# Performance work log

Hardware: AMD Instinct MI355X
Metric: run time of the kernel (lower is better)

## Reference

```python
import jax, jax.numpy as jnp
import numpy as np

DIM = 1024
N_HEADS = 16
WINDOW = 256
B, N = 16, 4096
ACC = 512
EPS = 1e-5


def setup_inputs() -> dict:
    key = jax.random.key(0)
    ks = jax.random.split(key, 16)
    D = DIM
    sc = 1.0 / np.sqrt(D)
    inp = {
        "x": jax.random.normal(ks[0], (B, N, D), dtype=jnp.float32),
        "state": jax.random.normal(ks[1], (B, D), dtype=jnp.float32),
        "acc_ctx": jax.random.normal(ks[2], (B, ACC, D), dtype=jnp.float32),
        "fix_pt": jax.random.randint(ks[3], (B,), 0, N, dtype=jnp.int32),
        # MultiheadAttention params (torch layout: in_proj_weight [3D, D])
        "in_proj_w": jax.random.normal(ks[4], (3 * D, D), dtype=jnp.float32) * sc,
        "in_proj_b": jnp.zeros((3 * D,), dtype=jnp.float32),
        "out_w": jax.random.normal(ks[5], (D, D), dtype=jnp.float32) * sc,
        "out_b": jnp.zeros((D,), dtype=jnp.float32),
        # LayerNorms
        "ln1_g": jnp.ones((D,), dtype=jnp.float32),
        "ln1_b": jnp.zeros((D,), dtype=jnp.float32),
        "ln2_g": jnp.ones((D,), dtype=jnp.float32),
        "ln2_b": jnp.zeros((D,), dtype=jnp.float32),
        # FFN: dim -> 4*dim -> dim (stored so that y = x @ w + b)
        "w1": jax.random.normal(ks[6], (D, 4 * D), dtype=jnp.float32) * sc,
        "b1": jnp.zeros((4 * D,), dtype=jnp.float32),
        "w2": jax.random.normal(ks[7], (4 * D, D), dtype=jnp.float32) * (1.0 / np.sqrt(4 * D)),
        "b2": jnp.zeros((D,), dtype=jnp.float32),
    }
    return inp


def _layer_norm(x, g, b):
    m = jnp.mean(x, axis=-1, keepdims=True)
    v = jnp.mean(jnp.square(x - m), axis=-1, keepdims=True)
    return (x - m) * jax.lax.rsqrt(v + EPS) * g + b


def _extract_windows(x, fix_pt):
    # Vectorized equivalent of the per-sample python loop. For even window_size
    # and N >= window_size the original logic reduces to a clamped start index.
    half = WINDOW // 2
    n = x.shape[1]
    start = jnp.clip(fix_pt - half, 0, n - WINDOW)  # [B]
    idx = start[:, None] + jnp.arange(WINDOW)       # [B, W]
    return jnp.take_along_axis(x, idx[:, :, None], axis=1)  # [B, W, D]


def _mha(xq, in_proj_w, in_proj_b, out_w, out_b):
    # torch nn.MultiheadAttention self-attention, batch_first
    Bq, L, D = xq.shape
    hd = D // N_HEADS
    qkv = xq @ in_proj_w.T + in_proj_b                     # [B, L, 3D]
    q, k, v = jnp.split(qkv, 3, axis=-1)
    def heads(t):
        return t.reshape(Bq, L, N_HEADS, hd).transpose(0, 2, 1, 3)  # [B,H,L,hd]
    q, k, v = heads(q), heads(k), heads(v)
    scores = jnp.einsum('bhqd,bhkd->bhqk', q, k) / np.sqrt(hd)
    attn = jax.nn.softmax(scores, axis=-1)
    o = jnp.einsum('bhqk,bhkd->bhqd', attn, v)             # [B,H,L,hd]
    o = o.transpose(0, 2, 1, 3).reshape(Bq, L, D)
    return o @ out_w.T + out_b


def reference(x, state, acc_ctx, in_proj_w, in_proj_b, out_w, out_b,
              ln1_g, ln1_b, ln2_g, ln2_b, w1, b1, w2, b2, fix_pt):
    window = _extract_windows(x, fix_pt)                   # [B, W, D]
    cls = state[:, None, :]                                # [B, 1, D]
    ctx = jnp.concatenate([cls, acc_ctx, window], axis=1)  # [B, 1+A+W, D]
    normed = _layer_norm(ctx, ln1_g, ln1_b)
    out = _mha(normed, in_proj_w, in_proj_b, out_w, out_b)
    ctx = ctx + out
    cls_out = ctx[:, 0]
    h = jax.nn.gelu(_layer_norm(cls_out, ln2_g, ln2_b) @ w1 + b1, approximate=False)
    cls_out = cls_out + h @ w2 + b2
    new_acc = jnp.concatenate([acc_ctx, window], axis=1)
    return cls_out, new_acc
```

## Files before the change

kernel.cpp:

```cpp
#include <hip/hip_runtime.h>
#include <hip/hip_bf16.h>
#include <math.h>

#define DIM 1024
#define NHEADS 16
#define HD 64
#define WIN 256
#define NB 16
#define NSEQ 4096
#define NACC 512
#define LCTX 769
#define MROWS 12304
#define MPAD2 12544
#define NKV 2048

typedef short bf16x8 __attribute__((ext_vector_type(8)));
typedef float f32x4 __attribute__((ext_vector_type(4)));

__device__ inline unsigned short f2b(float f) {
    union { float f; unsigned int u; } c; c.f = f;
    unsigned int u = c.u;
    u += 0x7FFFu + ((u >> 16) & 1u);
    return (unsigned short)(u >> 16);
}
__device__ inline float b2f(unsigned short h) {
    union { unsigned int u; float f; } c; c.u = ((unsigned int)h) << 16;
    return c.f;
}

__global__ __launch_bounds__(256) void build_ln_kernel(
    const float* __restrict__ x, const float* __restrict__ state,
    const float* __restrict__ acc_ctx, const int* __restrict__ fix_pt,
    const float* __restrict__ ln1_g, const float* __restrict__ ln1_b,
    unsigned short* __restrict__ normed, float* __restrict__ ctx0,
    float* __restrict__ newacc)
{
    int bid = blockIdx.x;
    int t = threadIdx.x;
    if (bid >= MROWS) {
        ushort4 z = make_ushort4(0, 0, 0, 0);
        ((ushort4*)(normed + (size_t)bid * DIM))[t] = z;
        return;
    }
    int b = bid / LCTX;
    int r = bid - b * LCTX;
    const float* src;
    if (r == 0) {
        src = state + (size_t)b * DIM;
    } else if (r <= NACC) {
        src = acc_ctx + ((size_t)b * NACC + (r - 1)) * DIM;
    } else {
        int fp = fix_pt[b];
        int start = fp - WIN / 2;
        if (start < 0) start = 0;
        if (start > NSEQ - WIN) start = NSEQ - WIN;
        src = x + ((size_t)b * NSEQ + start + (r - 1 - NACC)) * DIM;
    }
    float4 v = ((const float4*)src)[t];
    float s = v.x + v.y + v.z + v.w;
    float ss = v.x * v.x + v.y * v.y + v.z * v.z + v.w * v.w;
#pragma unroll
    for (int o = 32; o > 0; o >>= 1) { s += __shfl_down(s, o); ss += __shfl_down(ss, o); }
    __shared__ float rs[4], rss[4];
    int wid = t >> 6, lane = t & 63;
    if (lane == 0) { rs[wid] = s; rss[wid] = ss; }
    __syncthreads();
    float sum = rs[0] + rs[1] + rs[2] + rs[3];
    float sq  = rss[0] + rss[1] + rss[2] + rss[3];
    float mean = sum * (1.0f / DIM);
    float var = sq * (1.0f / DIM) - mean * mean;
    float rstd = rsqrtf(var + 1e-5f);
    float4 g  = ((const float4*)ln1_g)[t];
    float4 be = ((const float4*)ln1_b)[t];
    ushort4 nb;
    nb.x = f2b((v.x - mean) * rstd * g.x + be.x);
    nb.y = f2b((v.y - mean) * rstd * g.y + be.y);
    nb.z = f2b((v.z - mean) * rstd * g.z + be.z);
    nb.w = f2b((v.w - mean) * rstd * g.w + be.w);
    ((ushort4*)(normed + (size_t)bid * DIM))[t] = nb;
    if (r == 0) {
        ((float4*)(ctx0 + (size_t)b * DIM))[t] = v;
    } else {
        ((float4*)(newacc + ((size_t)b * (LCTX - 1) + (r - 1)) * DIM))[t] = v;
    }
}

__global__ __launch_bounds__(256) void convert_w_kernel(
    const float* __restrict__ w, unsigned short* __restrict__ wb, int n4)
{
    int idx = blockIdx.x * 256 + threadIdx.x;
    if (idx >= n4) return;
    float4 v = ((const float4*)w)[idx];
    ushort4 o;
    o.x = f2b(v.x); o.y = f2b(v.y); o.z = f2b(v.z); o.w = f2b(v.w);
    ((ushort4*)wb)[idx] = o;
}

__device__ inline void stage_half(const unsigned short* __restrict__ g,
                                  unsigned short* l, int t)
{
    {
        int r = t >> 3, c8 = (t & 7) ^ (r & 7);
        __builtin_amdgcn_global_load_lds(
            (const __attribute__((address_space(1))) void*)(g + (size_t)r * 1024 + c8 * 8),
            (__attribute__((address_space(3))) void*)(l + (size_t)t * 8), 16, 0, 0);
    }
    {
        int t2 = t + 512;
        int r = t2 >> 3, c8 = (t2 & 7) ^ (r & 7);
        __builtin_amdgcn_global_load_lds(
            (const __attribute__((address_space(1))) void*)(g + (size_t)r * 1024 + c8 * 8),
            (__attribute__((address_space(3))) void*)(l + (size_t)t2 * 8), 16, 0, 0);
    }
}

__device__ inline bf16x8 ldsw(const unsigned short* h, int r, int c8)
{
    int slot = r * 8 + (c8 ^ (r & 7));
    return *(const bf16x8*)(h + slot * 8);
}

__global__ __launch_bounds__(512, 2) void kv_gemm8_kernel(
    const unsigned short* __restrict__ A,
    const unsigned short* __restrict__ Bw,
    const float* __restrict__ bias,
    unsigned short* __restrict__ C)
{
    __shared__ unsigned short sh[2][2][2][128 * 64];
    const int mt = blockIdx.x, nt = blockIdx.y;
    const int t = threadIdx.x;
    const int wid = t >> 6, lane = t & 63;
    const int wm = wid >> 2, wn = wid & 3;
    const int l15 = lane & 15, l16 = lane >> 4;
    const int rB = (wn & 1) * 64;
    const unsigned short* Abase = A + (size_t)mt * 256 * 1024;
    const unsigned short* Bbase = Bw + (size_t)nt * 256 * 1024;

    f32x4 acc[8][4] = {};
    bf16x8 a[4][2], b[4][2];

    stage_half(Abase,                   &sh[0][0][0][0], t);
    stage_half(Abase + 128 * 1024,      &sh[0][0][1][0], t);
    stage_half(Bbase,                   &sh[0][1][0][0], t);
    stage_half(Bbase + 128 * 1024,      &sh[0][1][1][0], t);
    stage_half(Bbase + 64,              &sh[1][1][0][0], t);
    stage_half(Bbase + 128 * 1024 + 64, &sh[1][1][1][0], t);
    asm volatile("s_waitcnt vmcnt(4)" ::: "memory");
    __builtin_amdgcn_s_barrier();

    auto ktile = [&](int T, bool stA, bool stB, bool steady) {
        const int d = T & 1;
        const unsigned short* AH = &sh[d][0][wm][0];
        const unsigned short* BH = &sh[d][1][wn >> 1][0];
        const int kA = (T + 1) * 64;
        const int kB = (T + 2) * 64;

#pragma unroll
        for (int i = 0; i < 4; ++i) {
            a[i][0] = ldsw(AH, i * 16 + l15, l16);
            a[i][1] = ldsw(AH, i * 16 + l15, 4 + l16);
        }
#pragma unroll
        for (int j = 0; j < 2; ++j) {
            b[j][0] = ldsw(BH, rB + j * 16 + l15, l16);
            b[j][1] = ldsw(BH, rB + j * 16 + l15, 4 + l16);
        }
        if (stA) stage_half(Abase + kA, &sh[d ^ 1][0][0][0], t);
        __builtin_amdgcn_sched_barrier(0);
        __builtin_amdgcn_s_barrier();
        asm volatile("s_waitcnt lgkmcnt(0)" ::: "memory");
        __builtin_amdgcn_sched_barrier(0);
        __builtin_amdgcn_s_setprio(1);
#pragma unroll
        for (int i = 0; i < 4; ++i)
#pragma unroll
            for (int j = 0; j < 2; ++j) {
                acc[i][j] = __builtin_amdgcn_mfma_f32_16x16x32_bf16(a[i][0], b[j][0], acc[i][j], 0, 0, 0);
                acc[i][j] = __builtin_amdgcn_mfma_f32_16x16x32_bf16(a[i][1], b[j][1], acc[i][j], 0, 0, 0);
            }
        __builtin_amdgcn_s_setprio(0);
        __builtin_amdgcn_sched_barrier(0);
        __builtin_amdgcn_s_barrier();

#pragma unroll
        for (int j = 2; j < 4; ++j) {
            b[j][0] = ldsw(BH, rB + j * 16 + l15, l16);
            b[j][1] = ldsw(BH, rB + j * 16 + l15, 4 + l16);
        }
        if (stA) stage_half(Abase + 128 * 1024 + kA, &sh[d ^ 1][0][1][0], t);
        __builtin_amdgcn_sched_barrier(0);
        __builtin_amdgcn_s_barrier();
        asm volatile("s_waitcnt lgkmcnt(0)" ::: "memory");
        __builtin_amdgcn_sched_barrier(0);
        __builtin_amdgcn_s_setprio(1);
#pragma unroll
        for (int i = 0; i < 4; ++i)
#pragma unroll
            for (int j = 2; j < 4; ++j) {
                acc[i][j] = __builtin_amdgcn_mfma_f32_16x16x32_bf16(a[i][0], b[j][0], acc[i][j], 0, 0, 0);
                acc[i][j] = __builtin_amdgcn_mfma_f32_16x16x32_bf16(a[i][1], b[j][1], acc[i][j], 0, 0, 0);
            }
        __builtin_amdgcn_s_setprio(0);
        __builtin_amdgcn_sched_barrier(0);
        __builtin_amdgcn_s_barrier();

#pragma unroll
        for (int i = 0; i < 4; ++i) {
            a[i][0] = ldsw(AH, 64 + i * 16 + l15, l16);
            a[i][1] = ldsw(AH, 64 + i * 16 + l15, 4 + l16);
        }
        if (stB) stage_half(Bbase + kB, &sh[d][1][0][0], t);
        __builtin_amdgcn_sched_barrier(0);
        __builtin_amdgcn_s_barrier();
        asm volatile("s_waitcnt lgkmcnt(0)" ::: "memory");
        __builtin_amdgcn_sched_barrier(0);
        __builtin_amdgcn_s_setprio(1);
#pragma unroll
        for (int i = 0; i < 4; ++i)
#pragma unroll
            for (int j = 0; j < 2; ++j) {
                acc[4 + i][j] = __builtin_amdgcn_mfma_f32_16x16x32_bf16(a[i][0], b[j][0], acc[4 + i][j], 0, 0, 0);
                acc[4 + i][j] = __builtin_amdgcn_mfma_f32_16x16x32_bf16(a[i][1], b[j][1], acc[4 + i][j], 0, 0, 0);
            }
        __builtin_amdgcn_s_setprio(0);
        __builtin_amdgcn_sched_barrier(0);
        __builtin_amdgcn_s_barrier();

        if (stB) stage_half(Bbase + 128 * 1024 + kB, &sh[d][1][1][0], t);
        __builtin_amdgcn_sched_barrier(0);
        __builtin_amdgcn_s_barrier();
        asm volatile("s_waitcnt lgkmcnt(0)" ::: "memory");
        __builtin_amdgcn_sched_barrier(0);
        __builtin_amdgcn_s_setprio(1);
#pragma unroll
        for (int i = 0; i < 4; ++i)
#pragma unroll
            for (int j = 2; j < 4; ++j) {
                acc[4 + i][j] = __builtin_amdgcn_mfma_f32_16x16x32_bf16(a[i][0], b[j][0], acc[4 + i][j], 0, 0, 0);
                acc[4 + i][j] = __builtin_amdgcn_mfma_f32_16x16x32_bf16(a[i][1], b[j][1], acc[4 + i][j], 0, 0, 0);
            }
        __builtin_amdgcn_s_setprio(0);
        if (steady) {
            asm volatile("s_waitcnt vmcnt(4)" ::: "memory");
        } else {
            asm volatile("s_waitcnt vmcnt(0)" ::: "memory");
        }
        __builtin_amdgcn_sched_barrier(0);
        __builtin_amdgcn_s_barrier();
    };

    for (int T = 0; T < 14; ++T) ktile(T, true, true, true);
    ktile(14, true, false, false);
    ktile(15, false, false, false);

#pragma unroll
    for (int i = 0; i < 8; ++i) {
        int gmb = mt * 256 + wm * 128 + i * 16 + l16 * 4;
#pragma unroll
        for (int j = 0; j < 4; ++j) {
            int gn = nt * 256 + wn * 64 + j * 16 + l15;
            float bs = bias[gn];
#pragma unroll
            for (int r = 0; r < 4; ++r) {
                int gm = gmb + r;
                if (gm < MROWS) C[(size_t)gm * NKV + gn] = f2b(acc[i][j][r] + bs);
            }
        }
    }
}

__global__ __launch_bounds__(512) void attn_kernel(
    const unsigned short* __restrict__ normed,
    const unsigned short* __restrict__ Wq, const float* __restrict__ bq,
    const unsigned short* __restrict__ kv, float* __restrict__ o_all)
{
    int b = blockIdx.x >> 4, h = blockIdx.x & 15;
    int t = threadIdx.x;
    int wave = t >> 6, lane = t & 63;
    __shared__ float qs[64];
    __shared__ float sc[LCTX];
    __shared__ float red1[8], red2[8];
    __shared__ float po[8][64];

    {
        const unsigned short* nr = normed + (size_t)(b * LCTX) * DIM;
        bf16x8 n0 = *(const bf16x8*)(nr + lane * 16);
        bf16x8 n1 = *(const bf16x8*)(nr + lane * 16 + 8);
#pragma unroll
        for (int jj = 0; jj < 8; ++jj) {
            int d = wave * 8 + jj;
            const unsigned short* wr = Wq + (size_t)(h * 64 + d) * DIM;
            bf16x8 w0 = *(const bf16x8*)(wr + lane * 16);
            bf16x8 w1 = *(const bf16x8*)(wr + lane * 16 + 8);
            float s = 0.f;
#pragma unroll
            for (int u = 0; u < 8; ++u)
                s += b2f((unsigned short)n0[u]) * b2f((unsigned short)w0[u]);
#pragma unroll
            for (int u = 0; u < 8; ++u)
                s += b2f((unsigned short)n1[u]) * b2f((unsigned short)w1[u]);
#pragma unroll
            for (int o = 32; o > 0; o >>= 1) s += __shfl_down(s, o);
            if (lane == 0) qs[d] = s + bq[h * 64 + d];
        }
    }
    __syncthreads();

    float lmax = -1e30f;
    for (int l = t; l < LCTX; l += 512) {
        const unsigned short* kr = kv + ((size_t)(b * LCTX + l)) * NKV + h * 64;
        const uint4* k4 = (const uint4*)kr;
        float s = 0.f;
#pragma unroll
        for (int c = 0; c < 8; ++c) {
            uint4 u = k4[c];
            s += qs[c * 8 + 0] * b2f((unsigned short)(u.x & 0xffffu));
            s += qs[c * 8 + 1] * b2f((unsigned short)(u.x >> 16));
            s += qs[c * 8 + 2] * b2f((unsigned short)(u.y & 0xffffu));
            s += qs[c * 8 + 3] * b2f((unsigned short)(u.y >> 16));
            s += qs[c * 8 + 4] * b2f((unsigned short)(u.z & 0xffffu));
            s += qs[c * 8 + 5] * b2f((unsigned short)(u.z >> 16));
            s += qs[c * 8 + 6] * b2f((unsigned short)(u.w & 0xffffu));
            s += qs[c * 8 + 7] * b2f((unsigned short)(u.w >> 16));
        }
        s *= 0.125f;
        sc[l] = s;
        lmax = fmaxf(lmax, s);
    }
#pragma unroll
    for (int o = 32; o > 0; o >>= 1) lmax = fmaxf(lmax, __shfl_down(lmax, o));
    if (lane == 0) red1[wave] = lmax;
    __syncthreads();
    float m = red1[0];
#pragma unroll
    for (int w8 = 1; w8 < 8; ++w8) m = fmaxf(m, red1[w8]);

    float lsum = 0.f;
    for (int l = t; l < LCTX; l += 512) {
        float p = __expf(sc[l] - m);
        sc[l] = p;
        lsum += p;
    }
#pragma unroll
    for (int o = 32; o > 0; o >>= 1) lsum += __shfl_down(lsum, o);
    if (lane == 0) red2[wave] = lsum;
    __syncthreads();
    float S = 0.f;
#pragma unroll
    for (int w8 = 0; w8 < 8; ++w8) S += red2[w8];

    int rg = lane >> 3;
    int dc = (lane & 7) * 8;
    float acc[8] = {};
    for (int it = 0; it < 13; ++it) {
        int row = it * 64 + wave * 8 + rg;
        if (row < LCTX) {
            const unsigned short* vr =
                kv + ((size_t)(b * LCTX + row)) * NKV + 1024 + h * 64 + dc;
            bf16x8 v = *(const bf16x8*)vr;
            float p = sc[row];
#pragma unroll
            for (int u = 0; u < 8; ++u) acc[u] += p * b2f((unsigned short)v[u]);
        }
    }
#pragma unroll
    for (int u = 0; u < 8; ++u) {
        acc[u] += __shfl_xor(acc[u], 8);
        acc[u] += __shfl_xor(acc[u], 16);
        acc[u] += __shfl_xor(acc[u], 32);
    }
    if (rg == 0) {
#pragma unroll
        for (int u = 0; u < 8; ++u) po[wave][dc + u] = acc[u];
    }
    __syncthreads();
    if (t < 64) {
        float o = 0.f;
#pragma unroll
        for (int w8 = 0; w8 < 8; ++w8) o += po[w8][t];
        o_all[b * 1024 + h * 64 + t] = o / S;
    }
}

__global__ __launch_bounds__(256) void out_proj_kernel(
    const float* __restrict__ o_all, const float* __restrict__ out_w,
    const float* __restrict__ out_b, const float* __restrict__ ctx0,
    float* __restrict__ cls_pre)
{
    int gw = blockIdx.x * 4 + (threadIdx.x >> 6);
    int lane = threadIdx.x & 63;
    int b = gw >> 10, i = gw & 1023;
    const float* orow = o_all + (size_t)b * 1024;
    const float* wrow = out_w + (size_t)i * 1024;
    float s = 0.f;
#pragma unroll
    for (int kk = 0; kk < 16; ++kk) {
        int k = kk * 64 + lane;
        s += orow[k] * wrow[k];
    }
#pragma unroll
    for (int o = 32; o > 0; o >>= 1) s += __shfl_down(s, o);
    if (lane == 0) cls_pre[gw] = ctx0[gw] + s + out_b[i];
}

__global__ __launch_bounds__(256) void ln2_kernel(
    const float* __restrict__ cls_pre, const float* __restrict__ g,
    const float* __restrict__ be, const float* __restrict__ b2,
    float* __restrict__ ln2o, float* __restrict__ outp)
{
    int b = blockIdx.x, t = threadIdx.x;
    float4 v = ((const float4*)(cls_pre + (size_t)b * DIM))[t];
    float s = v.x + v.y + v.z + v.w;
    float ss = v.x * v.x + v.y * v.y + v.z * v.z + v.w * v.w;
#pragma unroll
    for (int o = 32; o > 0; o >>= 1) { s += __shfl_down(s, o); ss += __shfl_down(ss, o); }
    __shared__ float rs[4], rss[4];
    int wid = t >> 6, lane = t & 63;
    if (lane == 0) { rs[wid] = s; rss[wid] = ss; }
    __syncthreads();
    float sum = rs[0] + rs[1] + rs[2] + rs[3];
    float sq  = rss[0] + rss[1] + rss[2] + rss[3];
    float mean = sum * (1.0f / DIM);
    float var = sq * (1.0f / DIM) - mean * mean;
    float rstd = rsqrtf(var + 1e-5f);
    float4 gv = ((const float4*)g)[t];
    float4 bv = ((const float4*)be)[t];
    float4 o;
    o.x = (v.x - mean) * rstd * gv.x + bv.x;
    o.y = (v.y - mean) * rstd * gv.y + bv.y;
    o.z = (v.z - mean) * rstd * gv.z + bv.z;
    o.w = (v.w - mean) * rstd * gv.w + bv.w;
    ((float4*)(ln2o + (size_t)b * DIM))[t] = o;
    float4 b2v = ((const float4*)b2)[t];
    float4 oi;
    oi.x = v.x + b2v.x; oi.y = v.y + b2v.y; oi.z = v.z + b2v.z; oi.w = v.w + b2v.w;
    ((float4*)(outp + (size_t)b * DIM))[t] = oi;
}

__global__ __launch_bounds__(256) void mlp1p_kernel(
    const float* __restrict__ ln2v, const float* __restrict__ w1,
    float* __restrict__ part)
{
    __shared__ float l2s[16][256];
    __shared__ float red[4][64][16];
    int jc = blockIdx.x, kq = blockIdx.y;
    int t = threadIdx.x;
#pragma unroll
    for (int b = 0; b < 16; ++b)
        l2s[b][t] = ln2v[(size_t)b * 1024 + kq * 256 + t];
    __syncthreads();
    int jl = t & 63, ks = t >> 6;
    int j = jc * 64 + jl;
    float acc[16] = {};
    for (int kk = 0; kk < 64; ++kk) {
        int kl = ks * 64 + kk;
        float wv = w1[(size_t)(kq * 256 + kl) * 4096 + j];
#pragma unroll
        for (int b = 0; b < 16; ++b) acc[b] += l2s[b][kl] * wv;
    }
#pragma unroll
    for (int b = 0; b < 16; ++b) red[ks][jl][b] = acc[b];
    __syncthreads();
    int jl2 = t & 63, bq = t >> 6;
#pragma unroll
    for (int bb = 0; bb < 4; ++bb) {
        int b = bq * 4 + bb;
        float s = red[0][jl2][b] + red[1][jl2][b] + red[2][jl2][b] + red[3][jl2][b];
        part[((size_t)kq * 16 + b) * 4096 + jc * 64 + jl2] = s;
    }
}

__global__ __launch_bounds__(256) void mlp2a_kernel(
    const float* __restrict__ part, const float* __restrict__ b1,
    const float* __restrict__ w2, float* __restrict__ outp)
{
    __shared__ float hseg[16][256];
    __shared__ float red[4][64][16];
    int ic = blockIdx.x, kq = blockIdx.y;
    int t = threadIdx.x;
    {
        int j = kq * 256 + t;
        float bb1 = b1[j];
#pragma unroll
        for (int b = 0; b < 16; ++b) {
            float s = part[((size_t)0 * 16 + b) * 4096 + j]
                    + part[((size_t)1 * 16 + b) * 4096 + j]
                    + part[((size_t)2 * 16 + b) * 4096 + j]
                    + part[((size_t)3 * 16 + b) * 4096 + j];
            s += bb1;
            hseg[b][t] = 0.5f * s * (1.0f + erff(s * 0.70710678118f));
        }
    }
    __syncthreads();
    int il = t & 63, ks = t >> 6;
    int i = ic * 64 + il;
    float acc[16] = {};
    for (int kk = 0; kk < 64; ++kk) {
        int kl = ks * 64 + kk;
        float wv = w2[(size_t)(kq * 256 + kl) * 1024 + i];
#pragma unroll
        for (int b = 0; b < 16; ++b) acc[b] += hseg[b][kl] * wv;
    }
#pragma unroll
    for (int b = 0; b < 16; ++b) red[ks][il][b] = acc[b];
    __syncthreads();
    int il2 = t & 63, bq = t >> 6;
#pragma unroll
    for (int bb = 0; bb < 4; ++bb) {
        int b = bq * 4 + bb;
        float s = red[0][il2][b] + red[1][il2][b] + red[2][il2][b] + red[3][il2][b];
        atomicAdd(&outp[(size_t)b * 1024 + ic * 64 + il2], s);
    }
}

extern "C" void kernel_launch(void* const* d_in, const int* in_sizes, int n_in,
                              void* d_out, int out_size, void* d_ws, size_t ws_size,
                              hipStream_t stream)
{
    const float* x        = (const float*)d_in[0];
    const float* state    = (const float*)d_in[1];
    const float* acc_ctx  = (const float*)d_in[2];
    const int*   fix_pt   = (const int*)d_in[3];
    const float* in_proj_w = (const float*)d_in[4];
    const float* in_proj_b = (const float*)d_in[5];
    const float* out_w    = (const float*)d_in[6];
    const float* out_b    = (const float*)d_in[7];
    const float* ln1_g    = (const float*)d_in[8];
    const float* ln1_b    = (const float*)d_in[9];
    const float* ln2_g    = (const float*)d_in[10];
    const float* ln2_b    = (const float*)d_in[11];
    const float* w1       = (const float*)d_in[12];
    const float* b1       = (const float*)d_in[13];
    const float* w2       = (const float*)d_in[14];
    const float* b2       = (const float*)d_in[15];
    float* outp = (float*)d_out;

    char* ws = (char*)d_ws;
    unsigned short* normed = (unsigned short*)ws; ws += (size_t)MPAD2 * DIM * 2;
    unsigned short* Wb     = (unsigned short*)ws; ws += (size_t)3072 * DIM * 2;
    unsigned short* kvb    = (unsigned short*)ws; ws += (size_t)MROWS * NKV * 2;
    float* ctx0    = (float*)ws; ws += (size_t)NB * DIM * 4;
    float* o_all   = (float*)ws; ws += (size_t)NB * DIM * 4;
    float* cls_pre = (float*)ws; ws += (size_t)NB * DIM * 4;
    float* ln2v    = (float*)ws; ws += (size_t)NB * DIM * 4;
    float* part    = (float*)ws; ws += (size_t)4 * 16 * 4096 * 4;

    float* newacc = outp + (size_t)NB * DIM;

    hipLaunchKernelGGL(build_ln_kernel, dim3(MPAD2), dim3(256), 0, stream,
                       x, state, acc_ctx, fix_pt, ln1_g, ln1_b, normed, ctx0, newacc);
    hipLaunchKernelGGL(convert_w_kernel, dim3(3072), dim3(256), 0, stream,
                       in_proj_w, Wb, 3072 * DIM / 4);
    hipLaunchKernelGGL(kv_gemm8_kernel, dim3(49, 8), dim3(512), 0, stream,
                       normed, Wb + (size_t)1024 * DIM, in_proj_b + 1024, kvb);
    hipLaunchKernelGGL(attn_kernel, dim3(256), dim3(512), 0, stream,
                       normed, Wb, in_proj_b, kvb, o_all);
    hipLaunchKernelGGL(out_proj_kernel, dim3(4096), dim3(256), 0, stream,
                       o_all, out_w, out_b, ctx0, cls_pre);
    hipLaunchKernelGGL(ln2_kernel, dim3(16), dim3(256), 0, stream,
                       cls_pre, ln2_g, ln2_b, b2, ln2v, outp);
    hipLaunchKernelGGL(mlp1p_kernel, dim3(64, 4), dim3(256), 0, stream,
                       ln2v, w1, part);
    hipLaunchKernelGGL(mlp2a_kernel, dim3(16, 16), dim3(256), 0, stream,
                       part, b1, w2, outp);
}
```

Measured before the change: 166.9 us.

## Fuse weight conversion into LN launch and out-proj with LN2

Folds the in_proj weight bf16 conversion into the build_ln launch as extra blocks, and drops the separate convert kernel. Flattens the kv GEMM grid to 1D so the eight N-tiles of one M-tile are scheduled next to each other, which should improve reuse of A in cache. Merges out_proj and ln2 into one kernel with 16 blocks of 1024 threads, removing a launch and the cls_pre round trip. In exchange, each of those 16 blocks now streams all of out_w on its own, so the projection runs on only 16 CUs and may be bandwidth-limited.

Measured after the change: 200.5 us. +20.1%, slower.

```diff
diff --git a/kernel.cpp b/kernel.cpp
--- a/kernel.cpp
+++ b/kernel.cpp
@@ -32,11 +32,20 @@
     const float* __restrict__ x, const float* __restrict__ state,
     const float* __restrict__ acc_ctx, const int* __restrict__ fix_pt,
     const float* __restrict__ ln1_g, const float* __restrict__ ln1_b,
+    const float* __restrict__ in_proj_w, unsigned short* __restrict__ Wb,
     unsigned short* __restrict__ normed, float* __restrict__ ctx0,
     float* __restrict__ newacc)
 {
     int bid = blockIdx.x;
     int t = threadIdx.x;
+    if (bid >= MPAD2) {
+        int idx = (bid - MPAD2) * 256 + t;
+        float4 v = ((const float4*)in_proj_w)[idx];
+        ushort4 o;
+        o.x = f2b(v.x); o.y = f2b(v.y); o.z = f2b(v.z); o.w = f2b(v.w);
+        ((ushort4*)Wb)[idx] = o;
+        return;
+    }
     if (bid >= MROWS) {
         ushort4 z = make_ushort4(0, 0, 0, 0);
         ((ushort4*)(normed + (size_t)bid * DIM))[t] = z;
@@ -85,17 +94,6 @@
     }
 }
 
-__global__ __launch_bounds__(256) void convert_w_kernel(
-    const float* __restrict__ w, unsigned short* __restrict__ wb, int n4)
-{
-    int idx = blockIdx.x * 256 + threadIdx.x;
-    if (idx >= n4) return;
-    float4 v = ((const float4*)w)[idx];
-    ushort4 o;
-    o.x = f2b(v.x); o.y = f2b(v.y); o.z = f2b(v.z); o.w = f2b(v.w);
-    ((ushort4*)wb)[idx] = o;
-}
-
 __device__ inline void stage_half(const unsigned short* __restrict__ g,
                                   unsigned short* l, int t)
 {
@@ -127,7 +125,7 @@
     unsigned short* __restrict__ C)
 {
     __shared__ unsigned short sh[2][2][2][128 * 64];
-    const int mt = blockIdx.x, nt = blockIdx.y;
+    const int mt = blockIdx.x >> 3, nt = blockIdx.x & 7;
     const int t = threadIdx.x;
     const int wid = t >> 6, lane = t & 63;
     const int wm = wid >> 2, wn = wid & 3;
@@ -382,59 +380,51 @@
     }
 }
 
-__global__ __launch_bounds__(256) void out_proj_kernel(
+__global__ __launch_bounds__(1024) void opln2_kernel(
     const float* __restrict__ o_all, const float* __restrict__ out_w,
     const float* __restrict__ out_b, const float* __restrict__ ctx0,
-    float* __restrict__ cls_pre)
-{
-    int gw = blockIdx.x * 4 + (threadIdx.x >> 6);
-    int lane = threadIdx.x & 63;
-    int b = gw >> 10, i = gw & 1023;
-    const float* orow = o_all + (size_t)b * 1024;
-    const float* wrow = out_w + (size_t)i * 1024;
-    float s = 0.f;
-#pragma unroll
-    for (int kk = 0; kk < 16; ++kk) {
-        int k = kk * 64 + lane;
-        s += orow[k] * wrow[k];
-    }
-#pragma unroll
-    for (int o = 32; o > 0; o >>= 1) s += __shfl_down(s, o);
-    if (lane == 0) cls_pre[gw] = ctx0[gw] + s + out_b[i];
-}
-
-__global__ __launch_bounds__(256) void ln2_kernel(
-    const float* __restrict__ cls_pre, const float* __restrict__ g,
-    const float* __restrict__ be, const float* __restrict__ b2,
-    float* __restrict__ ln2o, float* __restrict__ outp)
+    const float* __restrict__ g, const float* __restrict__ be,
+    const float* __restrict__ b2, float* __restrict__ ln2o,
+    float* __restrict__ outp)
 {
     int b = blockIdx.x, t = threadIdx.x;
-    float4 v = ((const float4*)(cls_pre + (size_t)b * DIM))[t];
-    float s = v.x + v.y + v.z + v.w;
-    float ss = v.x * v.x + v.y * v.y + v.z * v.z + v.w * v.w;
+    int wave = t >> 6, lane = t & 63;
+    __shared__ float orow[1024];
+    __shared__ float dots[1024];
+    __shared__ float rs[16], rss[16];
+
+    orow[t] = o_all[(size_t)b * 1024 + t];
+    __syncthreads();
+
+    for (int jj = 0; jj < 64; ++jj) {
+        int i = wave * 64 + jj;
+        const float* wrow = out_w + (size_t)i * 1024;
+        float s = 0.f;
+#pragma unroll
+        for (int kk = 0; kk < 16; ++kk) {
+            int k = kk * 64 + lane;
+            s += orow[k] * wrow[k];
+        }
+#pragma unroll
+        for (int o = 32; o > 0; o >>= 1) s += __shfl_down(s, o);
+        if (lane == 0) dots[i] = s;
+    }
+    __syncthreads();
+
+    float v = ctx0[(size_t)b * 1024 + t] + dots[t] + out_b[t];
+    float s = v, ss = v * v;
 #pragma unroll
     for (int o = 32; o > 0; o >>= 1) { s += __shfl_down(s, o); ss += __shfl_down(ss, o); }
-    __shared__ float rs[4], rss[4];
-    int wid = t >> 6, lane = t & 63;
-    if (lane == 0) { rs[wid] = s; rss[wid] = ss; }
-    __syncthreads();
-    float sum = rs[0] + rs[1] + rs[2] + rs[3];
-    float sq  = rss[0] + rss[1] + rss[2] + rss[3];
+    if (lane == 0) { rs[wave] = s; rss[wave] = ss; }
+    __syncthreads();
+    float sum = 0.f, sq = 0.f;
+#pragma unroll
+    for (int w8 = 0; w8 < 16; ++w8) { sum += rs[w8]; sq += rss[w8]; }
     float mean = sum * (1.0f / DIM);
     float var = sq * (1.0f / DIM) - mean * mean;
     float rstd = rsqrtf(var + 1e-5f);
-    float4 gv = ((const float4*)g)[t];
-    float4 bv = ((const float4*)be)[t];
-    float4 o;
-    o.x = (v.x - mean) * rstd * gv.x + bv.x;
-    o.y = (v.y - mean) * rstd * gv.y + bv.y;
-    o.z = (v.z - mean) * rstd * gv.z + bv.z;
-    o.w = (v.w - mean) * rstd * gv.w + bv.w;
-    ((float4*)(ln2o + (size_t)b * DIM))[t] = o;
-    float4 b2v = ((const float4*)b2)[t];
-    float4 oi;
-    oi.x = v.x + b2v.x; oi.y = v.y + b2v.y; oi.z = v.z + b2v.z; oi.w = v.w + b2v.w;
-    ((float4*)(outp + (size_t)b * DIM))[t] = oi;
+    ln2o[(size_t)b * 1024 + t] = (v - mean) * rstd * g[t] + be[t];
+    outp[(size_t)b * 1024 + t] = v + b2[t];
 }
 
 __global__ __launch_bounds__(256) void mlp1p_kernel(
@@ -541,24 +531,20 @@
     unsigned short* kvb    = (unsigned short*)ws; ws += (size_t)MROWS * NKV * 2;
     float* ctx0    = (float*)ws; ws += (size_t)NB * DIM * 4;
     float* o_all   = (float*)ws; ws += (size_t)NB * DIM * 4;
-    float* cls_pre = (float*)ws; ws += (size_t)NB * DIM * 4;
     float* ln2v    = (float*)ws; ws += (size_t)NB * DIM * 4;
     float* part    = (float*)ws; ws += (size_t)4 * 16 * 4096 * 4;
 
     float* newacc = outp + (size_t)NB * DIM;
 
-    hipLaunchKernelGGL(build_ln_kernel, dim3(MPAD2), dim3(256), 0, stream,
-                       x, state, acc_ctx, fix_pt, ln1_g, ln1_b, normed, ctx0, newacc);
-    hipLaunchKernelGGL(convert_w_kernel, dim3(3072), dim3(256), 0, stream,
-                       in_proj_w, Wb, 3072 * DIM / 4);
-    hipLaunchKernelGGL(kv_gemm8_kernel, dim3(49, 8), dim3(512), 0, stream,
+    hipLaunchKernelGGL(build_ln_kernel, dim3(MPAD2 + 3072), dim3(256), 0, stream,
+                       x, state, acc_ctx, fix_pt, ln1_g, ln1_b,
+                       in_proj_w, Wb, normed, ctx0, newacc);
+    hipLaunchKernelGGL(kv_gemm8_kernel, dim3(392), dim3(512), 0, stream,
                        normed, Wb + (size_t)1024 * DIM, in_proj_b + 1024, kvb);
     hipLaunchKernelGGL(attn_kernel, dim3(256), dim3(512), 0, stream,
                        normed, Wb, in_proj_b, kvb, o_all);
-    hipLaunchKernelGGL(out_proj_kernel, dim3(4096), dim3(256), 0, stream,
-                       o_all, out_w, out_b, ctx0, cls_pre);
-    hipLaunchKernelGGL(ln2_kernel, dim3(16), dim3(256), 0, stream,
-                       cls_pre, ln2_g, ln2_b, b2, ln2v, outp);
+    hipLaunchKernelGGL(opln2_kernel, dim3(16), dim3(1024), 0, stream,
+                       o_all, out_w, out_b, ctx0, ln2_g, ln2_b, b2, ln2v, outp);
     hipLaunchKernelGGL(mlp1p_kernel, dim3(64, 4), dim3(256), 0, stream,
                        ln2v, w1, part);
     hipLaunchKernelGGL(mlp2a_kernel, dim3(16, 16), dim3(256), 0, stream,
```
